# Performance work log

Measured on AMD Instinct MI355X. Metric: run time of the kernel, lower is better.

## Reference

```python
import jax, jax.numpy as jnp
import numpy as np

B, T, E, H, V = 64, 21, 512, 512, 10000


def _lstm_step(x, h, c, W_ih, W_hh, b):
    # PyTorch LSTMCell gate order: i, f, g, o
    gates = x @ W_ih.T + h @ W_hh.T + b  # [B, 4H]
    i, f, g, o = jnp.split(gates, 4, axis=-1)
    i, f, o = jax.nn.sigmoid(i), jax.nn.sigmoid(f), jax.nn.sigmoid(o)
    g = jnp.tanh(g)
    c_new = f * c + i * g
    h_new = o * jnp.tanh(c_new)
    return h_new, c_new


def setup_inputs() -> dict:
    key = jax.random.key(0)
    ks = jax.random.split(key, 8)
    s_ih = 1.0 / np.sqrt(H)
    return {
        "features": jax.random.normal(ks[0], (B, E), jnp.float32),
        "caption_embedding": jax.random.normal(ks[1], (B, T, E), jnp.float32),
        "W_ih": jax.random.uniform(ks[2], (4 * H, E), jnp.float32, -s_ih, s_ih),
        "W_hh": jax.random.uniform(ks[3], (4 * H, H), jnp.float32, -s_ih, s_ih),
        "b_ih": jax.random.uniform(ks[4], (4 * H,), jnp.float32, -s_ih, s_ih),
        "b_hh": jax.random.uniform(ks[5], (4 * H,), jnp.float32, -s_ih, s_ih),
        "W_lin": jax.random.uniform(ks[6], (V, H), jnp.float32, -s_ih, s_ih),
        "b_lin": jax.random.uniform(ks[7], (V,), jnp.float32, -s_ih, s_ih),
    }


def reference(features, caption_embedding, W_ih, W_hh, b_ih, b_hh, W_lin, b_lin):
    b = b_ih + b_hh
    batch = features.shape[0]
    hidden = W_hh.shape[1]
    h0 = jnp.zeros((batch, hidden), features.dtype)
    c0 = jnp.zeros((batch, hidden), features.dtype)
    # t = 0: consume image features, no output emitted
    h, c = _lstm_step(features, h0, c0, W_ih, W_hh, b)
    # t = 1..T-1: consume caption_embedding[:, t-1], emit linear(h)
    emb_seq = jnp.swapaxes(caption_embedding[:, :-1, :], 0, 1)  # [T-1, B, E]

    def body(carry, x_t):
        h, c = carry
        h, c = _lstm_step(x_t, h, c, W_ih, W_hh, b)
        out = h @ W_lin.T + b_lin  # [B, V]
        return (h, c), out

    _, outs = jax.lax.scan(body, (h, c), emb_seq)  # [T-1, B, V]
    return jnp.swapaxes(outs, 0, 1)  # [B, T-1, V]
```

## Files before the change

kernel.cpp:

```cpp
#include <hip/hip_runtime.h>
#include <hip/hip_bf16.h>


#define NB 64
#define NT 21
#define NE 512
#define NH 512
#define NV 10000
#define G4 2048
#define FLGD 16

typedef __attribute__((ext_vector_type(8))) short bf16x8;
typedef __attribute__((ext_vector_type(4))) float f32x4;
typedef __attribute__((ext_vector_type(4))) unsigned short u16x4;

#define OFF_WIH_HI   0UL
#define OFF_WIH_LO   2097152UL
#define OFF_WLIN_HI  8388608UL
#define OFF_XSEQ_HI  18743296UL
#define OFF_XSEQ_LO  20185088UL
#define OFF_BIAS     21626880UL
#define OFF_XIH      21635072UL
#define OFF_GHH      32645120UL
#define OFF_GHL      32776192UL
#define OFF_C        32907264UL
#define OFF_CB       32950272UL
#define OFF_SLB      32993280UL
#define OFF_HBUF     33038336UL

__device__ inline unsigned short f2bf(float f) {
    unsigned int u = __float_as_uint(f);
    unsigned int r = u + 0x7FFFu + ((u >> 16) & 1u);
    return (unsigned short)(r >> 16);
}
__device__ inline float bf2f(unsigned short s) {
    return __uint_as_float(((unsigned int)s) << 16);
}

__device__ __forceinline__ void gl_lds16(const unsigned short* g, unsigned short* l) {
    auto gp = (const __attribute__((address_space(1))) unsigned int*)(unsigned long long)(const void*)g;
    auto lp = (__attribute__((address_space(3))) unsigned int*)(unsigned int)(unsigned long long)(void*)l;
    __builtin_amdgcn_global_load_lds(gp, lp, 16, 0, 0);
}

__device__ __forceinline__ void gl_lds16_sc(const unsigned short* g, unsigned short* l) {
    auto gp = (const __attribute__((address_space(1))) unsigned int*)(unsigned long long)(const void*)g;
    auto lp = (__attribute__((address_space(3))) unsigned int*)(unsigned int)(unsigned long long)(void*)l;
    __builtin_amdgcn_global_load_lds(gp, lp, 16, 0, 17);
}

__device__ __forceinline__ void st4_sc(unsigned int* p, unsigned int v) {
    asm volatile("global_store_dword %0, %1, off sc0 sc1" :: "v"(p), "v"(v) : "memory");
}
__device__ __forceinline__ void st8_sc(unsigned short* p, u16x4 v) {
    asm volatile("global_store_dwordx2 %0, %1, off sc0 sc1" :: "v"(p), "v"(v) : "memory");
}
__device__ __forceinline__ void st16_sc(float* p, f32x4 v) {
    asm volatile("global_store_dwordx4 %0, %1, off sc0 sc1" :: "v"(p), "v"(v) : "memory");
}

__global__ __launch_bounds__(512) void fused_all(
    const float* __restrict__ features, const float* __restrict__ cap,
    const float* __restrict__ W_ih_f, const float* __restrict__ W_hh_f,
    const float* __restrict__ b_ih, const float* __restrict__ b_hh,
    const float* __restrict__ W_lin_f, const float* __restrict__ b_lin,
    float* __restrict__ out, unsigned char* __restrict__ ws)
{
    __shared__ unsigned short Hhi[64 * 512];
    __shared__ unsigned short Hlo[64 * 512];
    __shared__ float glf[4096];
    const int tid = threadIdx.x;
    const int lane = tid & 63, wv = tid >> 6;
    const int mf = lane & 15, kg = lane >> 4;

    unsigned int* __restrict__ flgA = (unsigned int*)(ws + OFF_C);
    unsigned int* __restrict__ flgB = (unsigned int*)(ws + OFF_CB);
    unsigned int* __restrict__ slb  = (unsigned int*)(ws + OFF_SLB);
    unsigned short* __restrict__ hbuf = (unsigned short*)(ws + OFF_HBUF);
    const float* __restrict__ bias = (const float*)(ws + OFF_BIAS);
    float* __restrict__ xih_base = (float*)(ws + OFF_XIH);

    if (blockIdx.x < 32) {
        const int bc = blockIdx.x;
        const int q = wv & 3;
        const int mh = wv >> 2;

        unsigned short* __restrict__ ghh = (unsigned short*)(ws + OFF_GHH);
        unsigned short* __restrict__ ghl = (unsigned short*)(ws + OFF_GHL);

        bf16x8 bh[16], blo[16];
#pragma unroll
        for (int j = 0; j < 16; ++j) {
            const float* src = W_hh_f + (size_t)(q * 512 + bc * 16 + mf) * 512 + j * 32 + kg * 8;
            float4 w0 = *(const float4*)src;
            float4 w1 = *(const float4*)(src + 4);
            float ff[8] = {w0.x, w0.y, w0.z, w0.w, w1.x, w1.y, w1.z, w1.w};
#pragma unroll
            for (int e = 0; e < 8; ++e) {
                const unsigned short h = f2bf(ff[e]);
                bh[j][e] = (short)h;
                blo[j][e] = (short)f2bf(ff[e] - bf2f(h));
            }
        }

        const int crow = tid >> 3;
        const int cp = tid & 7;
        const int c0 = bc * 16 + cp * 2;
        const int jch = bc * 2 + (cp >> 2);
        const int sw = (jch * 64 + crow) * 8 + ((cp * 2) & 7);
        float creg0 = 0.f, creg1 = 0.f;

        float2 xp[4];
        auto load_xp = [&](int tt) {
            const float* __restrict__ xq = xih_base + (size_t)tt * NB * G4;
#pragma unroll
            for (int g2 = 0; g2 < 4; ++g2)
                xp[g2] = *(const float2*)&xq[crow * G4 + g2 * 512 + c0];
        };

        if (tid == 0) {
            while (__hip_atomic_load(&slb[0], __ATOMIC_RELAXED, __HIP_MEMORY_SCOPE_AGENT) < 16u)
                __builtin_amdgcn_s_sleep(1);
        }
        __syncthreads();
        load_xp(0);

        for (int t = 0; t < NT; ++t) {
            f32x4 acc[2];
            acc[0] = (f32x4){0.f, 0.f, 0.f, 0.f};
            acc[1] = (f32x4){0.f, 0.f, 0.f, 0.f};

            if (t > 0) {
                const int rd = (t + 1) & 1;
                const unsigned short* __restrict__ ghh_r = ghh + rd * (NB * NH);
                const unsigned short* __restrict__ ghl_r = ghl + rd * (NB * NH);

                {
                    const unsigned int* p = flgA + ((size_t)(t - 1) * 32 + bc) * FLGD;
                    unsigned int tgt = 0u;
                    if (lane < 4)       { p = flgA + ((size_t)(t - 1) * 32 + wv * 4 + lane) * FLGD; tgt = 1u; }
                    else if (lane == 4) { p = slb + (size_t)t * FLGD; tgt = 16u; }
                    while (__any(__hip_atomic_load(p, __ATOMIC_RELAXED, __HIP_MEMORY_SCOPE_AGENT) < tgt))
                        __builtin_amdgcn_s_sleep(1);
                }
                __builtin_amdgcn_sched_barrier(0);
#pragma unroll
                for (int pp = 0; pp < 4; ++pp) {
                    const int jj = (wv * 4 + pp) * 2;
                    gl_lds16_sc(ghh_r + (jj    ) * 512 + lane * 8, &Hhi[(jj    ) * 512 + lane * 8]);
                    gl_lds16_sc(ghh_r + (jj + 1) * 512 + lane * 8, &Hhi[(jj + 1) * 512 + lane * 8]);
                }
                __builtin_amdgcn_sched_barrier(0);
                {
                    const unsigned int* p = flgB + ((size_t)(t - 1) * 32 + bc) * FLGD;
                    unsigned int tgt = 0u;
                    if (lane < 4) { p = flgB + ((size_t)(t - 1) * 32 + wv * 4 + lane) * FLGD; tgt = 1u; }
                    while (__any(__hip_atomic_load(p, __ATOMIC_RELAXED, __HIP_MEMORY_SCOPE_AGENT) < tgt))
                        __builtin_amdgcn_s_sleep(1);
                }
                __builtin_amdgcn_sched_barrier(0);
#pragma unroll
                for (int pp = 0; pp < 4; ++pp) {
                    const int jj = (wv * 4 + pp) * 2;
                    gl_lds16_sc(ghl_r + (jj    ) * 512 + lane * 8, &Hlo[(jj    ) * 512 + lane * 8]);
                    gl_lds16_sc(ghl_r + (jj + 1) * 512 + lane * 8, &Hlo[(jj + 1) * 512 + lane * 8]);
                }
                __builtin_amdgcn_s_barrier();
                load_xp(t);
#pragma unroll
                for (int kt = 0; kt < 16; ++kt) {
                    const int j = kt * 4 + kg;
#pragma unroll
                    for (int m = 0; m < 2; ++m) {
                        const int row = mh * 32 + m * 16 + mf;
                        bf16x8 a_hi = *(const bf16x8*)&Hhi[(j * 64 + row) * 8];
                        acc[m] = __builtin_amdgcn_mfma_f32_16x16x32_bf16(a_hi, bh[kt], acc[m], 0, 0, 0);
                        acc[m] = __builtin_amdgcn_mfma_f32_16x16x32_bf16(a_hi, blo[kt], acc[m], 0, 0, 0);
                    }
                }
                asm volatile("s_waitcnt vmcnt(0)" ::: "memory");
                __builtin_amdgcn_s_barrier();
#pragma unroll
                for (int kt = 0; kt < 16; ++kt) {
                    const int j = kt * 4 + kg;
#pragma unroll
                    for (int m = 0; m < 2; ++m) {
                        const int row = mh * 32 + m * 16 + mf;
                        bf16x8 a_lo = *(const bf16x8*)&Hlo[(j * 64 + row) * 8];
                        acc[m] = __builtin_amdgcn_mfma_f32_16x16x32_bf16(a_lo, bh[kt], acc[m], 0, 0, 0);
                    }
                }
            }

#pragma unroll
            for (int m = 0; m < 2; ++m) {
                const int row = mh * 32 + m * 16 + kg * 4;
#pragma unroll
                for (int r = 0; r < 4; ++r)
                    glf[(q * 64 + row + r) * 16 + mf] = acc[m][r];
            }
            __syncthreads();

            {
                unsigned short* __restrict__ ghh_w = ghh + (t & 1) * (NB * NH);
                unsigned short* __restrict__ ghl_w = ghl + (t & 1) * (NB * NH);
                const float2 g0 = *(const float2*)&glf[(0 * 64 + crow) * 16 + cp * 2];
                const float2 g1 = *(const float2*)&glf[(1 * 64 + crow) * 16 + cp * 2];
                const float2 g2 = *(const float2*)&glf[(2 * 64 + crow) * 16 + cp * 2];
                const float2 g3 = *(const float2*)&glf[(3 * 64 + crow) * 16 + cp * 2];
                const float gi0 = g0.x + xp[0].x, gi1 = g0.y + xp[0].y;
                const float gf0 = g1.x + xp[1].x, gf1 = g1.y + xp[1].y;
                const float gg0 = g2.x + xp[2].x, gg1 = g2.y + xp[2].y;
                const float go0 = g3.x + xp[3].x, go1 = g3.y + xp[3].y;
                const float i0 = 1.f / (1.f + __expf(-gi0)), i1 = 1.f / (1.f + __expf(-gi1));
                const float f0 = 1.f / (1.f + __expf(-gf0)), f1 = 1.f / (1.f + __expf(-gf1));
                const float ga0 = tanhf(gg0),                ga1 = tanhf(gg1);
                const float o0 = 1.f / (1.f + __expf(-go0)), o1 = 1.f / (1.f + __expf(-go1));
                const float cn0 = f0 * creg0 + i0 * ga0;
                const float cn1 = f1 * creg1 + i1 * ga1;
                creg0 = cn0; creg1 = cn1;
                const float h0 = o0 * tanhf(cn0);
                const float h1 = o1 * tanhf(cn1);
                const unsigned short hi0 = f2bf(h0), hi1 = f2bf(h1);
                const unsigned short lo0 = f2bf(h0 - bf2f(hi0)), lo1 = f2bf(h1 - bf2f(hi1));
                const unsigned int hpack = (unsigned int)hi0 | ((unsigned int)hi1 << 16);
                const unsigned int lpack = (unsigned int)lo0 | ((unsigned int)lo1 << 16);
                st4_sc((unsigned int*)&ghh_w[sw], hpack);
                st4_sc((unsigned int*)&ghl_w[sw], lpack);
                const int sl = (t == 0) ? 0 : t - 1;
                st4_sc((unsigned int*)&hbuf[(size_t)sl * (NB * NH) + crow * NH + c0], hpack);
            }

            asm volatile("s_waitcnt vmcnt(2)" ::: "memory");
            __builtin_amdgcn_s_barrier();
            if (tid == 0) st4_sc(flgA + ((size_t)t * 32 + bc) * FLGD, 1u);
            asm volatile("s_waitcnt vmcnt(0)" ::: "memory");
            __builtin_amdgcn_s_barrier();
            if (tid == 0) st4_sc(flgB + ((size_t)t * 32 + bc) * FLGD, 1u);
        }
        asm volatile("s_waitcnt vmcnt(0)" ::: "memory");
        return;
    }

    const int g = blockIdx.x - 32;
    const int mw2 = (wv >> 2) * 32, nw2 = (wv & 3) * 32;

    {
        unsigned short* wih_hi = (unsigned short*)(ws + OFF_WIH_HI);
        unsigned short* wih_lo = (unsigned short*)(ws + OFF_WIH_LO);
        unsigned short* xs_hi = (unsigned short*)(ws + OFF_XSEQ_HI);
        unsigned short* xs_lo = (unsigned short*)(ws + OFF_XSEQ_LO);
        float* bias_w = (float*)(ws + OFF_BIAS);
        int idx = g * 512 + tid;
        for (int it = 0; it < 4; ++it, idx += 114688) {
            if (idx < 262144) {
                const int i4 = idx * 4;
                float4 w = *(const float4*)(W_ih_f + i4);
                u16x4 hi, lo;
                hi.x = f2bf(w.x); lo.x = f2bf(w.x - bf2f(hi.x));
                hi.y = f2bf(w.y); lo.y = f2bf(w.y - bf2f(hi.y));
                hi.z = f2bf(w.z); lo.z = f2bf(w.z - bf2f(hi.z));
                hi.w = f2bf(w.w); lo.w = f2bf(w.w - bf2f(hi.w));
                st8_sc(wih_hi + i4, hi);
                st8_sc(wih_lo + i4, lo);
            } else if (idx < 434176) {
                const int i4 = (idx - 262144) * 4;
                const int e = i4 & 511;
                const int b = (i4 >> 9) & 63;
                const int t2 = i4 >> 15;
                float4 x = (t2 == 0) ? *(const float4*)(features + b * NE + e)
                                     : *(const float4*)(cap + b * (NT * NE) + (t2 - 1) * NE + e);
                u16x4 hi, lo;
                hi.x = f2bf(x.x); lo.x = f2bf(x.x - bf2f(hi.x));
                hi.y = f2bf(x.y); lo.y = f2bf(x.y - bf2f(hi.y));
                hi.z = f2bf(x.z); lo.z = f2bf(x.z - bf2f(hi.z));
                hi.w = f2bf(x.w); lo.w = f2bf(x.w - bf2f(hi.w));
                st8_sc(xs_hi + i4, hi);
                st8_sc(xs_lo + i4, lo);
            } else if (idx < 434688) {
                const int j = (idx - 434176) * 4;
                float4 a = *(const float4*)(b_ih + j);
                float4 b = *(const float4*)(b_hh + j);
                f32x4 s;
                s[0] = a.x + b.x; s[1] = a.y + b.y; s[2] = a.z + b.z; s[3] = a.w + b.w;
                st16_sc(bias_w + j, s);
            }
        }
        asm volatile("s_waitcnt vmcnt(0)" ::: "memory");
        __syncthreads();
        if (tid == 0) {
            __hip_atomic_fetch_add(&slb[24 * FLGD], 1u, __ATOMIC_RELAXED, __HIP_MEMORY_SCOPE_AGENT);
            while (__hip_atomic_load(&slb[24 * FLGD], __ATOMIC_RELAXED, __HIP_MEMORY_SCOPE_AGENT) < 224u)
                __builtin_amdgcn_s_sleep(1);
        }
        __syncthreads();
    }

    {
        const unsigned short* __restrict__ xh = (const unsigned short*)(ws + OFF_XSEQ_HI);
        const unsigned short* __restrict__ xl = (const unsigned short*)(ws + OFF_XSEQ_LO);
        const unsigned short* __restrict__ wih_h = (const unsigned short*)(ws + OFF_WIH_HI);
        const unsigned short* __restrict__ wih_l = (const unsigned short*)(ws + OFF_WIH_LO);

        unsigned short* Ah2 = Hhi;
        unsigned short* Al2 = Hhi + 4096;
        unsigned short* Bh2 = Hhi + 8192;
        unsigned short* Bl2 = Hhi + 16384;

        const int ntile = (g < 112) ? 2 : 1;
        for (int p = 0; p < ntile; ++p) {
            const int T = (p == 0) ? g : 224 + g;
            const int slab = T >> 4, ct = T & 15;
            const unsigned short* __restrict__ xhA = xh + (size_t)slab * 64 * 512;
            const unsigned short* __restrict__ xlA = xl + (size_t)slab * 64 * 512;

            auto stageA = [&](int buf, int k0) {
                if (tid < 256) {
                    const int s = tid, r = s >> 2, kc = (s & 3) * 8;
                    gl_lds16(xhA + (size_t)r * 512 + k0 + kc, &Ah2[buf * 2048 + s * 8]);
                    gl_lds16(xlA + (size_t)r * 512 + k0 + kc, &Al2[buf * 2048 + s * 8]);
                } else {
#pragma unroll
                    for (int h2 = 0; h2 < 2; ++h2) {
                        const int s = h2 * 256 + (tid - 256), r = s >> 2, kc = (s & 3) * 8;
                        gl_lds16(wih_h + (size_t)(ct * 128 + r) * 512 + k0 + kc, &Bh2[buf * 4096 + s * 8]);
                        gl_lds16(wih_l + (size_t)(ct * 128 + r) * 512 + k0 + kc, &Bl2[buf * 4096 + s * 8]);
                    }
                }
            };

            f32x4 acc2[2][2];
#pragma unroll
            for (int i = 0; i < 2; i++)
#pragma unroll
                for (int j = 0; j < 2; j++) acc2[i][j] = (f32x4){0.f, 0.f, 0.f, 0.f};

            stageA(0, 0);
            for (int kt = 0; kt < 16; ++kt) {
                __syncthreads();
                const int cur = kt & 1;
                if (kt < 15) stageA(cur ^ 1, (kt + 1) * 32);
                bf16x8 ah_[2], al_[2], bh_[2], bl_[2];
#pragma unroll
                for (int i = 0; i < 2; i++) {
                    ah_[i] = *(const bf16x8*)&Ah2[cur * 2048 + (mw2 + i * 16 + mf) * 32 + kg * 8];
                    al_[i] = *(const bf16x8*)&Al2[cur * 2048 + (mw2 + i * 16 + mf) * 32 + kg * 8];
                    bh_[i] = *(const bf16x8*)&Bh2[cur * 4096 + (nw2 + i * 16 + mf) * 32 + kg * 8];
                    bl_[i] = *(const bf16x8*)&Bl2[cur * 4096 + (nw2 + i * 16 + mf) * 32 + kg * 8];
                }
#pragma unroll
                for (int i = 0; i < 2; i++)
#pragma unroll
                    for (int j = 0; j < 2; j++) {
                        acc2[i][j] = __builtin_amdgcn_mfma_f32_16x16x32_bf16(ah_[i], bh_[j], acc2[i][j], 0, 0, 0);
                        acc2[i][j] = __builtin_amdgcn_mfma_f32_16x16x32_bf16(ah_[i], bl_[j], acc2[i][j], 0, 0, 0);
                        acc2[i][j] = __builtin_amdgcn_mfma_f32_16x16x32_bf16(al_[i], bh_[j], acc2[i][j], 0, 0, 0);
                    }
            }
#pragma unroll
            for (int i = 0; i < 2; i++)
#pragma unroll
                for (int j = 0; j < 2; j++) {
                    const int col = ct * 128 + nw2 + j * 16 + mf;
                    const float bb = bias[col];
#pragma unroll
                    for (int r = 0; r < 4; r++) {
                        const int row = slab * 64 + mw2 + i * 16 + kg * 4 + r;
                        st4_sc((unsigned int*)&xih_base[(size_t)row * G4 + col],
                               __float_as_uint(acc2[i][j][r] + bb));
                    }
                }
            asm volatile("s_waitcnt vmcnt(0)" ::: "memory");
            __syncthreads();
            if (tid == 0)
                __hip_atomic_fetch_add(&slb[slab * FLGD], 1u, __ATOMIC_RELAXED, __HIP_MEMORY_SCOPE_AGENT);
            __syncthreads();
        }
    }

    {
        unsigned short* wlin_w = (unsigned short*)(ws + OFF_WLIN_HI);
        int idx = g * 512 + tid;
        for (int it = 0; it < 12; ++it, idx += 114688) {
            if (idx < 1280000) {
                const int i4 = idx * 4;
                float4 w = *(const float4*)(W_lin_f + i4);
                u16x4 hi;
                hi.x = f2bf(w.x); hi.y = f2bf(w.y); hi.z = f2bf(w.z); hi.w = f2bf(w.w);
                st8_sc(wlin_w + i4, hi);
            }
        }
        asm volatile("s_waitcnt vmcnt(0)" ::: "memory");
        __syncthreads();
        if (tid == 0) {
            __hip_atomic_fetch_add(&slb[25 * FLGD], 1u, __ATOMIC_RELAXED, __HIP_MEMORY_SCOPE_AGENT);
            while (__hip_atomic_load(&slb[25 * FLGD], __ATOMIC_RELAXED, __HIP_MEMORY_SCOPE_AGENT) < 224u)
                __builtin_amdgcn_s_sleep(1);
        }
        __syncthreads();
    }

    const unsigned short* __restrict__ wlin = (const unsigned short*)(ws + OFF_WLIN_HI);
    const int jt = g % 79;
    const int rshare = g / 79;
    const int nshare = (jt < 66) ? 3 : 2;
    const int n0g = jt * 128;

    unsigned short* __restrict__ AsB = Hhi;
    unsigned short* __restrict__ BsB = Hhi + 4096;

    for (int tt = rshare; tt < NT - 1; tt += nshare) {
        if (wv == 0) {
            const unsigned int* fp = flgB + ((size_t)(tt + 1) * 32 + (lane & 31)) * FLGD;
            while (__hip_atomic_load(fp, __ATOMIC_RELAXED, __HIP_MEMORY_SCOPE_AGENT) == 0u)
                __builtin_amdgcn_s_sleep(2);
        }
        __syncthreads();

        const unsigned short* __restrict__ hbA = hbuf + (size_t)tt * (NB * NH);
        auto stageC = [&](int buf, int k0) {
            if (tid < 256) {
                const int s = tid;
                const int r = s >> 2, kcol = (s & 3) * 8;
                gl_lds16_sc(hbA + (size_t)r * 512 + k0 + kcol, &AsB[buf * 2048 + s * 8]);
            } else {
#pragma unroll
                for (int h2 = 0; h2 < 2; ++h2) {
                    const int s = h2 * 256 + (tid - 256);
                    const int r = s >> 2, kcol = (s & 3) * 8;
                    gl_lds16(wlin + (size_t)(n0g + r) * 512 + k0 + kcol, &BsB[buf * 4096 + s * 8]);
                }
            }
        };

        f32x4 acc2[2][2];
#pragma unroll
        for (int i = 0; i < 2; i++)
#pragma unroll
            for (int j = 0; j < 2; j++) acc2[i][j] = (f32x4){0.f, 0.f, 0.f, 0.f};

        stageC(0, 0);
        for (int kt = 0; kt < 16; ++kt) {
            __syncthreads();
            const int cur = kt & 1;
            if (kt < 15) stageC(cur ^ 1, (kt + 1) * 32);
            bf16x8 af[2], bfv[2];
#pragma unroll
            for (int i = 0; i < 2; i++) {
                af[i]  = *(const bf16x8*)&AsB[cur * 2048 + (mw2 + i * 16 + mf) * 32 + kg * 8];
                bfv[i] = *(const bf16x8*)&BsB[cur * 4096 + (nw2 + i * 16 + mf) * 32 + kg * 8];
            }
#pragma unroll
            for (int i = 0; i < 2; i++)
#pragma unroll
                for (int j = 0; j < 2; j++)
                    acc2[i][j] = __builtin_amdgcn_mfma_f32_16x16x32_bf16(af[i], bfv[j], acc2[i][j], 0, 0, 0);
        }
#pragma unroll
        for (int i = 0; i < 2; i++)
#pragma unroll
            for (int j = 0; j < 2; j++) {
                const int col = n0g + nw2 + j * 16 + mf;
                if (col < NV) {
                    const float bl = b_lin[col];
#pragma unroll
                    for (int r = 0; r < 4; r++) {
                        const int b_ = mw2 + i * 16 + kg * 4 + r;
                        out[(size_t)b_ * ((NT - 1) * NV) + (size_t)tt * NV + col] = acc2[i][j][r] + bl;
                    }
                }
            }
        __syncthreads();
    }
}

extern "C" void kernel_launch(void* const* d_in, const int* in_sizes, int n_in,
                              void* d_out, int out_size, void* d_ws, size_t ws_size,
                              hipStream_t stream)
{
    const float* features = (const float*)d_in[0];
    const float* cap      = (const float*)d_in[1];
    const float* W_ih     = (const float*)d_in[2];
    const float* W_hh     = (const float*)d_in[3];
    const float* b_ih     = (const float*)d_in[4];
    const float* b_hh     = (const float*)d_in[5];
    const float* W_lin    = (const float*)d_in[6];
    const float* b_lin    = (const float*)d_in[7];
    float* out = (float*)d_out;
    unsigned char* ws = (unsigned char*)d_ws;

    (void)hipMemsetAsync(ws + OFF_C, 0, 87680, stream);

    hipLaunchKernelGGL(fused_all, dim3(256), dim3(512), 0, stream,
                       features, cap, W_ih, W_hh, b_ih, b_hh, W_lin, b_lin, out, ws);
}
```

Baseline: 259.9 us.

## Merge per-step flags into per-wave atomic counter and split MFMA accumulators

Replaces the two-phase flag handshake (flgA after hi stores, flgB after lo stores, each gated by block barriers) with a single counter per block and step. Each wave atomically increments it after draining its own stores, and consumers wait for a count of 8, removing two block barriers per recurrent step. MFMA chains are split into three independent accumulators to shorten dependency chains, and tanhf is replaced with an exp-based fast tanh. The risks are slightly different rounding from the fast tanh and the loss of early overlap, since consumers now wait for both hi and lo halves before loading either.

```diff
diff --git a/kernel.cpp b/kernel.cpp
--- a/kernel.cpp
+++ b/kernel.cpp
@@ -24,8 +24,7 @@
 #define OFF_GHH      32645120UL
 #define OFF_GHL      32776192UL
 #define OFF_C        32907264UL
-#define OFF_CB       32950272UL
-#define OFF_SLB      32993280UL
+#define OFF_SLB      32950272UL
 #define OFF_HBUF     33038336UL
 
 __device__ inline unsigned short f2bf(float f) {
@@ -35,6 +34,11 @@
 }
 __device__ inline float bf2f(unsigned short s) {
     return __uint_as_float(((unsigned int)s) << 16);
+}
+__device__ inline float tanhf_fast(float x) {
+    float xc = fminf(20.f, fmaxf(-20.f, x));
+    float e = __expf(2.f * xc);
+    return (e - 1.f) / (e + 1.f);
 }
 
 __device__ __forceinline__ void gl_lds16(const unsigned short* g, unsigned short* l) {
@@ -73,8 +77,7 @@
     const int lane = tid & 63, wv = tid >> 6;
     const int mf = lane & 15, kg = lane >> 4;
 
-    unsigned int* __restrict__ flgA = (unsigned int*)(ws + OFF_C);
-    unsigned int* __restrict__ flgB = (unsigned int*)(ws + OFF_CB);
+    unsigned int* __restrict__ flgC = (unsigned int*)(ws + OFF_C);
     unsigned int* __restrict__ slb  = (unsigned int*)(ws + OFF_SLB);
     unsigned short* __restrict__ hbuf = (unsigned short*)(ws + OFF_HBUF);
     const float* __restrict__ bias = (const float*)(ws + OFF_BIAS);
@@ -126,9 +129,13 @@
         load_xp(0);
 
         for (int t = 0; t < NT; ++t) {
-            f32x4 acc[2];
-            acc[0] = (f32x4){0.f, 0.f, 0.f, 0.f};
-            acc[1] = (f32x4){0.f, 0.f, 0.f, 0.f};
+            f32x4 accA[2], accB[2], accC[2];
+#pragma unroll
+            for (int m = 0; m < 2; ++m) {
+                accA[m] = (f32x4){0.f, 0.f, 0.f, 0.f};
+                accB[m] = (f32x4){0.f, 0.f, 0.f, 0.f};
+                accC[m] = (f32x4){0.f, 0.f, 0.f, 0.f};
+            }
 
             if (t > 0) {
                 const int rd = (t + 1) & 1;
@@ -136,9 +143,9 @@
                 const unsigned short* __restrict__ ghl_r = ghl + rd * (NB * NH);
 
                 {
-                    const unsigned int* p = flgA + ((size_t)(t - 1) * 32 + bc) * FLGD;
+                    const unsigned int* p = flgC + ((size_t)(t - 1) * 32 + bc) * FLGD;
                     unsigned int tgt = 0u;
-                    if (lane < 4)       { p = flgA + ((size_t)(t - 1) * 32 + wv * 4 + lane) * FLGD; tgt = 1u; }
+                    if (lane < 4)       { p = flgC + ((size_t)(t - 1) * 32 + wv * 4 + lane) * FLGD; tgt = 8u; }
                     else if (lane == 4) { p = slb + (size_t)t * FLGD; tgt = 16u; }
                     while (__any(__hip_atomic_load(p, __ATOMIC_RELAXED, __HIP_MEMORY_SCOPE_AGENT) < tgt))
                         __builtin_amdgcn_s_sleep(1);
@@ -150,21 +157,13 @@
                     gl_lds16_sc(ghh_r + (jj    ) * 512 + lane * 8, &Hhi[(jj    ) * 512 + lane * 8]);
                     gl_lds16_sc(ghh_r + (jj + 1) * 512 + lane * 8, &Hhi[(jj + 1) * 512 + lane * 8]);
                 }
-                __builtin_amdgcn_sched_barrier(0);
-                {
-                    const unsigned int* p = flgB + ((size_t)(t - 1) * 32 + bc) * FLGD;
-                    unsigned int tgt = 0u;
-                    if (lane < 4) { p = flgB + ((size_t)(t - 1) * 32 + wv * 4 + lane) * FLGD; tgt = 1u; }
-                    while (__any(__hip_atomic_load(p, __ATOMIC_RELAXED, __HIP_MEMORY_SCOPE_AGENT) < tgt))
-                        __builtin_amdgcn_s_sleep(1);
-                }
-                __builtin_amdgcn_sched_barrier(0);
 #pragma unroll
                 for (int pp = 0; pp < 4; ++pp) {
                     const int jj = (wv * 4 + pp) * 2;
                     gl_lds16_sc(ghl_r + (jj    ) * 512 + lane * 8, &Hlo[(jj    ) * 512 + lane * 8]);
                     gl_lds16_sc(ghl_r + (jj + 1) * 512 + lane * 8, &Hlo[(jj + 1) * 512 + lane * 8]);
                 }
+                asm volatile("s_waitcnt vmcnt(8)" ::: "memory");
                 __builtin_amdgcn_s_barrier();
                 load_xp(t);
 #pragma unroll
@@ -174,8 +173,8 @@
                     for (int m = 0; m < 2; ++m) {
                         const int row = mh * 32 + m * 16 + mf;
                         bf16x8 a_hi = *(const bf16x8*)&Hhi[(j * 64 + row) * 8];
-                        acc[m] = __builtin_amdgcn_mfma_f32_16x16x32_bf16(a_hi, bh[kt], acc[m], 0, 0, 0);
-                        acc[m] = __builtin_amdgcn_mfma_f32_16x16x32_bf16(a_hi, blo[kt], acc[m], 0, 0, 0);
+                        accA[m] = __builtin_amdgcn_mfma_f32_16x16x32_bf16(a_hi, bh[kt], accA[m], 0, 0, 0);
+                        accB[m] = __builtin_amdgcn_mfma_f32_16x16x32_bf16(a_hi, blo[kt], accB[m], 0, 0, 0);
                     }
                 }
                 asm volatile("s_waitcnt vmcnt(0)" ::: "memory");
@@ -187,17 +186,18 @@
                     for (int m = 0; m < 2; ++m) {
                         const int row = mh * 32 + m * 16 + mf;
                         bf16x8 a_lo = *(const bf16x8*)&Hlo[(j * 64 + row) * 8];
-                        acc[m] = __builtin_amdgcn_mfma_f32_16x16x32_bf16(a_lo, bh[kt], acc[m], 0, 0, 0);
+                        accC[m] = __builtin_amdgcn_mfma_f32_16x16x32_bf16(a_lo, bh[kt], accC[m], 0, 0, 0);
                     }
                 }
             }
 
 #pragma unroll
             for (int m = 0; m < 2; ++m) {
+                f32x4 acc = (accA[m] + accB[m]) + accC[m];
                 const int row = mh * 32 + m * 16 + kg * 4;
 #pragma unroll
                 for (int r = 0; r < 4; ++r)
-                    glf[(q * 64 + row + r) * 16 + mf] = acc[m][r];
+                    glf[(q * 64 + row + r) * 16 + mf] = acc[r];
             }
             __syncthreads();
 
@@ -214,13 +214,13 @@
                 const float go0 = g3.x + xp[3].x, go1 = g3.y + xp[3].y;
                 const float i0 = 1.f / (1.f + __expf(-gi0)), i1 = 1.f / (1.f + __expf(-gi1));
                 const float f0 = 1.f / (1.f + __expf(-gf0)), f1 = 1.f / (1.f + __expf(-gf1));
-                const float ga0 = tanhf(gg0),                ga1 = tanhf(gg1);
+                const float ga0 = tanhf_fast(gg0),           ga1 = tanhf_fast(gg1);
                 const float o0 = 1.f / (1.f + __expf(-go0)), o1 = 1.f / (1.f + __expf(-go1));
                 const float cn0 = f0 * creg0 + i0 * ga0;
                 const float cn1 = f1 * creg1 + i1 * ga1;
                 creg0 = cn0; creg1 = cn1;
-                const float h0 = o0 * tanhf(cn0);
-                const float h1 = o1 * tanhf(cn1);
+                const float h0 = o0 * tanhf_fast(cn0);
+                const float h1 = o1 * tanhf_fast(cn1);
                 const unsigned short hi0 = f2bf(h0), hi1 = f2bf(h1);
                 const unsigned short lo0 = f2bf(h0 - bf2f(hi0)), lo1 = f2bf(h1 - bf2f(hi1));
                 const unsigned int hpack = (unsigned int)hi0 | ((unsigned int)hi1 << 16);
@@ -231,12 +231,10 @@
                 st4_sc((unsigned int*)&hbuf[(size_t)sl * (NB * NH) + crow * NH + c0], hpack);
             }
 
-            asm volatile("s_waitcnt vmcnt(2)" ::: "memory");
-            __builtin_amdgcn_s_barrier();
-            if (tid == 0) st4_sc(flgA + ((size_t)t * 32 + bc) * FLGD, 1u);
             asm volatile("s_waitcnt vmcnt(0)" ::: "memory");
-            __builtin_amdgcn_s_barrier();
-            if (tid == 0) st4_sc(flgB + ((size_t)t * 32 + bc) * FLGD, 1u);
+            if (lane == 0)
+                __hip_atomic_fetch_add(flgC + ((size_t)t * 32 + bc) * FLGD, 1u,
+                                       __ATOMIC_RELAXED, __HIP_MEMORY_SCOPE_AGENT);
         }
         asm volatile("s_waitcnt vmcnt(0)" ::: "memory");
         return;
@@ -411,8 +409,8 @@
 
     for (int tt = rshare; tt < NT - 1; tt += nshare) {
         if (wv == 0) {
-            const unsigned int* fp = flgB + ((size_t)(tt + 1) * 32 + (lane & 31)) * FLGD;
-            while (__hip_atomic_load(fp, __ATOMIC_RELAXED, __HIP_MEMORY_SCOPE_AGENT) == 0u)
+            const unsigned int* fp = flgC + ((size_t)(tt + 1) * 32 + (lane & 31)) * FLGD;
+            while (__hip_atomic_load(fp, __ATOMIC_RELAXED, __HIP_MEMORY_SCOPE_AGENT) < 8u)
                 __builtin_amdgcn_s_sleep(2);
         }
         __syncthreads();
@@ -489,7 +487,7 @@
     float* out = (float*)d_out;
     unsigned char* ws = (unsigned char*)d_ws;
 
-    (void)hipMemsetAsync(ws + OFF_C, 0, 87680, stream);
+    (void)hipMemsetAsync(ws + OFF_C, 0, 44672, stream);
 
     hipLaunchKernelGGL(fused_all, dim3(256), dim3(512), 0, stream,
                        features, cap, W_ih, W_hh, b_ih, b_hh, W_lin, b_lin, out, ws);
```

Result: slower. 276.2 us (+6.3%).

## Split operand prep into separate kernel, split MFMA accumulators, fast tanh

Applied to the files above, without the earlier changes.

Moves the bf16 hi/lo splitting of W_ih, the input sequence and the bias sum out of the persistent fused kernel into its own launch. This removes the in-kernel 224-block spin barrier and the sc0/sc1 stores, at the cost of an extra kernel launch. The recurrent MFMA chain now uses three independent accumulators instead of one serial chain, to cut dependency stalls. tanhf is replaced by an exp-based fast tanh, which may shift accuracy slightly.

```diff
diff --git a/kernel.cpp b/kernel.cpp
--- a/kernel.cpp
+++ b/kernel.cpp
@@ -36,6 +36,11 @@
 __device__ inline float bf2f(unsigned short s) {
     return __uint_as_float(((unsigned int)s) << 16);
 }
+__device__ inline float tanhf_fast(float x) {
+    float xc = fminf(20.f, fmaxf(-20.f, x));
+    float e = __expf(2.f * xc);
+    return (e - 1.f) / (e + 1.f);
+}
 
 __device__ __forceinline__ void gl_lds16(const unsigned short* g, unsigned short* l) {
     auto gp = (const __attribute__((address_space(1))) unsigned int*)(unsigned long long)(const void*)g;
@@ -55,16 +60,55 @@
 __device__ __forceinline__ void st8_sc(unsigned short* p, u16x4 v) {
     asm volatile("global_store_dwordx2 %0, %1, off sc0 sc1" :: "v"(p), "v"(v) : "memory");
 }
-__device__ __forceinline__ void st16_sc(float* p, f32x4 v) {
-    asm volatile("global_store_dwordx4 %0, %1, off sc0 sc1" :: "v"(p), "v"(v) : "memory");
+
+__global__ __launch_bounds__(256) void prep_kernel(
+    const float* __restrict__ features, const float* __restrict__ cap,
+    const float* __restrict__ W_ih, const float* __restrict__ b_ih,
+    const float* __restrict__ b_hh, unsigned char* __restrict__ ws)
+{
+    const int idx = blockIdx.x * 256 + threadIdx.x;
+    unsigned short* wih_hi = (unsigned short*)(ws + OFF_WIH_HI);
+    unsigned short* wih_lo = (unsigned short*)(ws + OFF_WIH_LO);
+    unsigned short* xs_hi = (unsigned short*)(ws + OFF_XSEQ_HI);
+    unsigned short* xs_lo = (unsigned short*)(ws + OFF_XSEQ_LO);
+    float* bias = (float*)(ws + OFF_BIAS);
+
+    if (idx < 262144) {
+        const int i4 = idx * 4;
+        float4 w = *(const float4*)(W_ih + i4);
+        u16x4 hi, lo;
+        hi.x = f2bf(w.x); lo.x = f2bf(w.x - bf2f(hi.x));
+        hi.y = f2bf(w.y); lo.y = f2bf(w.y - bf2f(hi.y));
+        hi.z = f2bf(w.z); lo.z = f2bf(w.z - bf2f(hi.z));
+        hi.w = f2bf(w.w); lo.w = f2bf(w.w - bf2f(hi.w));
+        *(u16x4*)(wih_hi + i4) = hi;
+        *(u16x4*)(wih_lo + i4) = lo;
+    } else if (idx < 434176) {
+        const int i4 = (idx - 262144) * 4;
+        const int e = i4 & 511;
+        const int b = (i4 >> 9) & 63;
+        const int t = i4 >> 15;
+        float4 x = (t == 0) ? *(const float4*)(features + b * NE + e)
+                            : *(const float4*)(cap + b * (NT * NE) + (t - 1) * NE + e);
+        u16x4 hi, lo;
+        hi.x = f2bf(x.x); lo.x = f2bf(x.x - bf2f(hi.x));
+        hi.y = f2bf(x.y); lo.y = f2bf(x.y - bf2f(hi.y));
+        hi.z = f2bf(x.z); lo.z = f2bf(x.z - bf2f(hi.z));
+        hi.w = f2bf(x.w); lo.w = f2bf(x.w - bf2f(hi.w));
+        *(u16x4*)(xs_hi + i4) = hi;
+        *(u16x4*)(xs_lo + i4) = lo;
+    } else if (idx < 434688) {
+        const int j = (idx - 434176) * 4;
+        float4 a = *(const float4*)(b_ih + j);
+        float4 b = *(const float4*)(b_hh + j);
+        *(float4*)(bias + j) = make_float4(a.x + b.x, a.y + b.y, a.z + b.z, a.w + b.w);
+    }
 }
 
 __global__ __launch_bounds__(512) void fused_all(
-    const float* __restrict__ features, const float* __restrict__ cap,
-    const float* __restrict__ W_ih_f, const float* __restrict__ W_hh_f,
-    const float* __restrict__ b_ih, const float* __restrict__ b_hh,
-    const float* __restrict__ W_lin_f, const float* __restrict__ b_lin,
-    float* __restrict__ out, unsigned char* __restrict__ ws)
+    const float* __restrict__ W_hh_f, const float* __restrict__ W_lin_f,
+    const float* __restrict__ b_lin, float* __restrict__ out,
+    unsigned char* __restrict__ ws)
 {
     __shared__ unsigned short Hhi[64 * 512];
     __shared__ unsigned short Hlo[64 * 512];
@@ -126,9 +170,13 @@
         load_xp(0);
 
         for (int t = 0; t < NT; ++t) {
-            f32x4 acc[2];
-            acc[0] = (f32x4){0.f, 0.f, 0.f, 0.f};
-            acc[1] = (f32x4){0.f, 0.f, 0.f, 0.f};
+            f32x4 accA[2], accB[2], accC[2];
+#pragma unroll
+            for (int m = 0; m < 2; ++m) {
+                accA[m] = (f32x4){0.f, 0.f, 0.f, 0.f};
+                accB[m] = (f32x4){0.f, 0.f, 0.f, 0.f};
+                accC[m] = (f32x4){0.f, 0.f, 0.f, 0.f};
+            }
 
             if (t > 0) {
                 const int rd = (t + 1) & 1;
@@ -174,8 +222,8 @@
                     for (int m = 0; m < 2; ++m) {
                         const int row = mh * 32 + m * 16 + mf;
                         bf16x8 a_hi = *(const bf16x8*)&Hhi[(j * 64 + row) * 8];
-                        acc[m] = __builtin_amdgcn_mfma_f32_16x16x32_bf16(a_hi, bh[kt], acc[m], 0, 0, 0);
-                        acc[m] = __builtin_amdgcn_mfma_f32_16x16x32_bf16(a_hi, blo[kt], acc[m], 0, 0, 0);
+                        accA[m] = __builtin_amdgcn_mfma_f32_16x16x32_bf16(a_hi, bh[kt], accA[m], 0, 0, 0);
+                        accB[m] = __builtin_amdgcn_mfma_f32_16x16x32_bf16(a_hi, blo[kt], accB[m], 0, 0, 0);
                     }
                 }
                 asm volatile("s_waitcnt vmcnt(0)" ::: "memory");
@@ -187,17 +235,18 @@
                     for (int m = 0; m < 2; ++m) {
                         const int row = mh * 32 + m * 16 + mf;
                         bf16x8 a_lo = *(const bf16x8*)&Hlo[(j * 64 + row) * 8];
-                        acc[m] = __builtin_amdgcn_mfma_f32_16x16x32_bf16(a_lo, bh[kt], acc[m], 0, 0, 0);
+                        accC[m] = __builtin_amdgcn_mfma_f32_16x16x32_bf16(a_lo, bh[kt], accC[m], 0, 0, 0);
                     }
                 }
             }
 
 #pragma unroll
             for (int m = 0; m < 2; ++m) {
+                f32x4 acc = (accA[m] + accB[m]) + accC[m];
                 const int row = mh * 32 + m * 16 + kg * 4;
 #pragma unroll
                 for (int r = 0; r < 4; ++r)
-                    glf[(q * 64 + row + r) * 16 + mf] = acc[m][r];
+                    glf[(q * 64 + row + r) * 16 + mf] = acc[r];
             }
             __syncthreads();
 
@@ -214,13 +263,13 @@
                 const float go0 = g3.x + xp[3].x, go1 = g3.y + xp[3].y;
                 const float i0 = 1.f / (1.f + __expf(-gi0)), i1 = 1.f / (1.f + __expf(-gi1));
                 const float f0 = 1.f / (1.f + __expf(-gf0)), f1 = 1.f / (1.f + __expf(-gf1));
-                const float ga0 = tanhf(gg0),                ga1 = tanhf(gg1);
+                const float ga0 = tanhf_fast(gg0),           ga1 = tanhf_fast(gg1);
                 const float o0 = 1.f / (1.f + __expf(-go0)), o1 = 1.f / (1.f + __expf(-go1));
                 const float cn0 = f0 * creg0 + i0 * ga0;
                 const float cn1 = f1 * creg1 + i1 * ga1;
                 creg0 = cn0; creg1 = cn1;
-                const float h0 = o0 * tanhf(cn0);
-                const float h1 = o1 * tanhf(cn1);
+                const float h0 = o0 * tanhf_fast(cn0);
+                const float h1 = o1 * tanhf_fast(cn1);
                 const unsigned short hi0 = f2bf(h0), hi1 = f2bf(h1);
                 const unsigned short lo0 = f2bf(h0 - bf2f(hi0)), lo1 = f2bf(h1 - bf2f(hi1));
                 const unsigned int hpack = (unsigned int)hi0 | ((unsigned int)hi1 << 16);
@@ -244,57 +293,6 @@
 
     const int g = blockIdx.x - 32;
     const int mw2 = (wv >> 2) * 32, nw2 = (wv & 3) * 32;
-
-    {
-        unsigned short* wih_hi = (unsigned short*)(ws + OFF_WIH_HI);
-        unsigned short* wih_lo = (unsigned short*)(ws + OFF_WIH_LO);
-        unsigned short* xs_hi = (unsigned short*)(ws + OFF_XSEQ_HI);
-        unsigned short* xs_lo = (unsigned short*)(ws + OFF_XSEQ_LO);
-        float* bias_w = (float*)(ws + OFF_BIAS);
-        int idx = g * 512 + tid;
-        for (int it = 0; it < 4; ++it, idx += 114688) {
-            if (idx < 262144) {
-                const int i4 = idx * 4;
-                float4 w = *(const float4*)(W_ih_f + i4);
-                u16x4 hi, lo;
-                hi.x = f2bf(w.x); lo.x = f2bf(w.x - bf2f(hi.x));
-                hi.y = f2bf(w.y); lo.y = f2bf(w.y - bf2f(hi.y));
-                hi.z = f2bf(w.z); lo.z = f2bf(w.z - bf2f(hi.z));
-                hi.w = f2bf(w.w); lo.w = f2bf(w.w - bf2f(hi.w));
-                st8_sc(wih_hi + i4, hi);
-                st8_sc(wih_lo + i4, lo);
-            } else if (idx < 434176) {
-                const int i4 = (idx - 262144) * 4;
-                const int e = i4 & 511;
-                const int b = (i4 >> 9) & 63;
-                const int t2 = i4 >> 15;
-                float4 x = (t2 == 0) ? *(const float4*)(features + b * NE + e)
-                                     : *(const float4*)(cap + b * (NT * NE) + (t2 - 1) * NE + e);
-                u16x4 hi, lo;
-                hi.x = f2bf(x.x); lo.x = f2bf(x.x - bf2f(hi.x));
-                hi.y = f2bf(x.y); lo.y = f2bf(x.y - bf2f(hi.y));
-                hi.z = f2bf(x.z); lo.z = f2bf(x.z - bf2f(hi.z));
-                hi.w = f2bf(x.w); lo.w = f2bf(x.w - bf2f(hi.w));
-                st8_sc(xs_hi + i4, hi);
-                st8_sc(xs_lo + i4, lo);
-            } else if (idx < 434688) {
-                const int j = (idx - 434176) * 4;
-                float4 a = *(const float4*)(b_ih + j);
-                float4 b = *(const float4*)(b_hh + j);
-                f32x4 s;
-                s[0] = a.x + b.x; s[1] = a.y + b.y; s[2] = a.z + b.z; s[3] = a.w + b.w;
-                st16_sc(bias_w + j, s);
-            }
-        }
-        asm volatile("s_waitcnt vmcnt(0)" ::: "memory");
-        __syncthreads();
-        if (tid == 0) {
-            __hip_atomic_fetch_add(&slb[24 * FLGD], 1u, __ATOMIC_RELAXED, __HIP_MEMORY_SCOPE_AGENT);
-            while (__hip_atomic_load(&slb[24 * FLGD], __ATOMIC_RELAXED, __HIP_MEMORY_SCOPE_AGENT) < 224u)
-                __builtin_amdgcn_s_sleep(1);
-        }
-        __syncthreads();
-    }
 
     {
         const unsigned short* __restrict__ xh = (const unsigned short*)(ws + OFF_XSEQ_HI);
@@ -491,6 +489,8 @@
 
     (void)hipMemsetAsync(ws + OFF_C, 0, 87680, stream);
 
+    hipLaunchKernelGGL(prep_kernel, dim3(1698), dim3(256), 0, stream,
+                       features, cap, W_ih, b_ih, b_hh, ws);
     hipLaunchKernelGGL(fused_all, dim3(256), dim3(512), 0, stream,
-                       features, cap, W_ih, W_hh, b_ih, b_hh, W_lin, b_lin, out, ws);
-}
+                       W_hh, W_lin, b_lin, out, ws);
+}
```

Result: faster. 246.1 us (-5.3%).
